# Performance work log

Measured on AMD Instinct MI355X. Metric: run time of the kernel, lower is better.

Reference implementation:

```python
import jax, jax.numpy as jnp
import numpy as np

COMMIT = 0.25
DECAY = 0.99
EPS = 1e-5
TEMP = 0.1
B, T, D, M = 32, 512, 256, 1024


def setup_inputs() -> dict:
    key = jax.random.key(0)
    k1, k2, k3 = jax.random.split(key, 3)
    init_bound = 1.0 / 400.0
    audio = jax.random.normal(k1, (B, T, D), jnp.float32)
    video = jax.random.normal(k2, (B, T, D), jnp.float32)
    embedding = jax.random.uniform(k3, (M, D), jnp.float32, -init_bound, init_bound)
    return {
        "audio_semantic": audio,
        "video_semantic": video,
        "embedding": embedding,
        "ema_count": jnp.zeros((M,), jnp.float32),
        "ema_weight": embedding,
        "epoch": 1,
    }


def reference(audio_semantic, video_semantic, embedding, ema_count, ema_weight, epoch):
    sg = jax.lax.stop_gradient
    Bc, Tc, Dc = audio_semantic.shape
    Mc = embedding.shape[0]

    a_flat = sg(audio_semantic.reshape(-1, Dc))  # [N, D], detached in torch
    v_flat = sg(video_semantic.reshape(-1, Dc))

    e_sq = jnp.sum(embedding ** 2, axis=1)  # [M]

    def sq_dist(x):
        return e_sq[None, :] + jnp.sum(x ** 2, axis=1, keepdims=True) - 2.0 * (x @ embedding.T)

    a_dist = sq_dist(a_flat)
    v_dist = sq_dist(v_flat)
    a_dist_g = sq_dist(audio_semantic.reshape(-1, Dc))  # grad-carrying copies
    v_dist_g = sq_dist(video_semantic.reshape(-1, Dc))

    # soft assignment probs and entropy-based adjustment
    a_ph = jax.nn.softmax(-jnp.sqrt(jnp.maximum(a_dist_g, 0.0)), axis=1)
    v_ph = jax.nn.softmax(-jnp.sqrt(jnp.maximum(v_dist_g, 0.0)), axis=1)
    entropy = lambda p: -jnp.sum(p * jnp.log(p + 1e-5), axis=-1)
    max_entropy = float(np.log(Mc))
    a_adj = (1.0 - entropy(a_ph) / max_entropy)[:, None]  # [N, 1]
    v_adj = (1.0 - entropy(v_ph) / max_entropy)[:, None]

    # hard assignment
    a_idx = jnp.argmin(a_dist, axis=-1)  # [N]
    v_idx = jnp.argmin(v_dist, axis=-1)
    a_onehot = jax.nn.one_hot(a_idx, Mc, dtype=jnp.float32)  # a_positive
    v_onehot = jax.nn.one_hot(v_idx, Mc, dtype=jnp.float32)  # v_positive
    a_enc = sg(a_adj * a_onehot)  # detached entropy-weighted encodings
    v_enc = sg(v_adj * v_onehot)

    # EMA update pass 1 (video-driven)
    ec = DECAY * ema_count + (1.0 - DECAY) * jnp.sum(v_enc, axis=0)
    n = jnp.sum(ec)
    ec = (ec + EPS) / (n + Mc * EPS) * n
    ew = DECAY * ema_weight + 0.5 * (1.0 - DECAY) * (v_enc.T @ (v_flat + a_flat))
    # EMA update pass 2 (audio-driven)
    ec = DECAY * ec + (1.0 - DECAY) * jnp.sum(a_enc, axis=0)
    n = jnp.sum(ec)
    ec = (ec + EPS) / (n + Mc * EPS) * n
    ew = DECAY * ew + 0.5 * (1.0 - DECAY) * (a_enc.T @ (a_flat + v_flat))
    emb_new = sg(ew / ec[:, None])  # updated codebook used by the contrastive loss

    en = emb_new / jnp.maximum(jnp.linalg.norm(emb_new, axis=1, keepdims=True), 1e-8)

    def info_nce(feats, self_pos, coupled_pos):
        fn = feats / jnp.maximum(jnp.linalg.norm(feats, axis=1, keepdims=True), 1e-8)
        logp = jax.nn.log_softmax((fn @ en.T) / TEMP, axis=1)  # [N, M]
        ce = lambda tgt: -jnp.mean(jnp.sum(tgt * logp, axis=1))
        return COMMIT * ce(self_pos) + (1.0 - COMMIT) * ce(coupled_pos)

    a_cpcl = info_nce(audio_semantic.reshape(-1, Dc), a_onehot, v_onehot)
    v_cpcl = info_nce(video_semantic.reshape(-1, Dc), v_onehot, a_onehot)
    cpcl_loss = (COMMIT * a_cpcl + COMMIT * v_cpcl) / Bc
    return cpcl_loss
```

## Files before the change

### kernel.cpp

```cpp
#include <hip/hip_runtime.h>
#include <math.h>

#define NROWS 16384
#define NR2 32768
#define DIM 256
#define MC 1024
#define GBM 128
#define GBK 64
#define NCHUNK 16

constexpr float kDecay = 0.99f;
constexpr float kEps = 1e-5f;
constexpr float kTemp = 0.1f;
constexpr float kCommit = 0.25f;
constexpr float kMaxEnt = 6.93147180559945f;

using short8 = __attribute__((ext_vector_type(8))) short;
using f32x4 = __attribute__((ext_vector_type(4))) float;

__device__ __forceinline__ float wave_sum(float v) {
#pragma unroll
  for (int off = 32; off > 0; off >>= 1) v += __shfl_xor(v, off);
  return v;
}

__device__ __forceinline__ unsigned short f2bf(float f) {
  union { float f; unsigned int u; } c;
  c.f = f;
  const unsigned int u = c.u;
  return (unsigned short)((u + 0x7FFFu + ((u >> 16) & 1u)) >> 16);
}
__device__ __forceinline__ float bf2f(unsigned short h) {
  union { unsigned int u; float f; } c;
  c.u = ((unsigned int)h) << 16;
  return c.f;
}

__global__ __launch_bounds__(256) void convert_all(const float* __restrict__ A,
                                                   const float* __restrict__ V,
                                                   const float* __restrict__ E,
                                                   unsigned short* __restrict__ av_bf,
                                                   unsigned short* __restrict__ e_bf,
                                                   float* __restrict__ xsq,
                                                   float* __restrict__ esq) {
  const int row = (int)((blockIdx.x * blockDim.x + threadIdx.x) >> 6);
  const int lane = threadIdx.x & 63;
  const float* src;
  unsigned short* dst;
  float* sqo;
  if (row < NR2) {
    src = (row < NROWS) ? (A + (size_t)row * DIM) : (V + (size_t)(row - NROWS) * DIM);
    dst = av_bf + (size_t)row * DIM;
    sqo = xsq + row;
  } else {
    const int r = row - NR2;
    src = E + (size_t)r * DIM;
    dst = e_bf + (size_t)r * DIM;
    sqo = esq + r;
  }
  const float4 x = *reinterpret_cast<const float4*>(src + (lane << 2));
  float s = x.x * x.x + x.y * x.y + x.z * x.z + x.w * x.w;
  ushort4 b;
  b.x = f2bf(x.x); b.y = f2bf(x.y); b.z = f2bf(x.z); b.w = f2bf(x.w);
  *reinterpret_cast<ushort4*>(dst + (lane << 2)) = b;
  s = wave_sum(s);
  if (lane == 0) *sqo = s;
}

__device__ __forceinline__ void stage_tile(const unsigned short* __restrict__ X,
                                           const unsigned short* __restrict__ W,
                                           char* lds, int k0, int row0, int col0, int w, int l) {
#pragma unroll
  for (int j = 0; j < 4; ++j) {
    const int sbase = __builtin_amdgcn_readfirstlane((w * 4 + j) * 1024);
    const int s = sbase + (l << 4);
    const int row = s >> 7;
    const int colb = s & 127;
    const int scolb = colb ^ ((row & 7) << 4);
    const char* srcA = (const char*)(X + (size_t)(row0 + row) * DIM + k0) + scolb;
    const char* srcB = (const char*)(W + (size_t)(col0 + row) * DIM + k0) + scolb;
    __builtin_amdgcn_global_load_lds(
        (const __attribute__((address_space(1))) unsigned int*)srcA,
        (__attribute__((address_space(3))) unsigned int*)(lds + sbase), 16, 0, 0);
    __builtin_amdgcn_global_load_lds(
        (const __attribute__((address_space(1))) unsigned int*)srcB,
        (__attribute__((address_space(3))) unsigned int*)(lds + 16384 + sbase), 16, 0, 0);
  }
}

__device__ __forceinline__ void mfma_step(const char* lds, f32x4 acc[4][4], int wr, int wc,
                                          int l) {
#pragma unroll
  for (int ks = 0; ks < 2; ++ks) {
    short8 af[4], bq[4];
    const int cb = ks * 64 + (l >> 4) * 16;
#pragma unroll
    for (int m = 0; m < 4; ++m) {
      const int ar = wr * 64 + m * 16 + (l & 15);
      af[m] = *reinterpret_cast<const short8*>(lds + ar * 128 + (cb ^ ((ar & 7) << 4)));
    }
#pragma unroll
    for (int n = 0; n < 4; ++n) {
      const int br = wc * 64 + n * 16 + (l & 15);
      bq[n] = *reinterpret_cast<const short8*>(lds + 16384 + br * 128 + (cb ^ ((br & 7) << 4)));
    }
#pragma unroll
    for (int m = 0; m < 4; ++m)
#pragma unroll
      for (int n = 0; n < 4; ++n)
        acc[m][n] = __builtin_amdgcn_mfma_f32_16x16x32_bf16(bq[n], af[m], acc[m][n], 0, 0, 0);
  }
}

__global__ __launch_bounds__(256, 4) void gemm_dist(const unsigned short* __restrict__ X,
                                                    const unsigned short* __restrict__ W,
                                                    const float* __restrict__ xsq,
                                                    const float* __restrict__ esq,
                                                    float4* __restrict__ pd4) {
  __shared__ __align__(16) char lds[32768 + 1024];
  float* esq_s = (float*)(lds + 32768);
  float* xsq_s = (float*)(lds + 32768 + 512);
  const int tid = threadIdx.x;
  const int l = tid & 63;
  const int w = tid >> 6;
  const int wr = w >> 1, wc = w & 1;
  int bid = blockIdx.y * 8 + blockIdx.x;
  bid = (bid & 7) * 256 + (bid >> 3);
  const int bx = bid & 7;
  const int by = bid >> 3;
  const int row0 = by * GBM;
  const int col0 = bx * GBM;
  if (tid < 128) esq_s[tid] = esq[col0 + tid];
  else xsq_s[tid - 128] = xsq[row0 + tid - 128];
  f32x4 acc[4][4] = {};
#pragma unroll
  for (int t = 0; t < 4; ++t) {
    stage_tile(X, W, lds, t * GBK, row0, col0, w, l);
    __syncthreads();
    mfma_step(lds, acc, wr, wc, l);
    if (t < 3) __syncthreads();
  }
  const int l15 = l & 15, lg = l >> 4;
  const int chunk = bx * 2 + wc;
#pragma unroll
  for (int m = 0; m < 4; ++m) {
    const float xs = xsq_s[wr * 64 + m * 16 + l15];
    float se = 0.f, wsabs = 0.f, bv = INFINITY;
    int bi = 0;
#pragma unroll
    for (int n = 0; n < 4; ++n) {
      const f32x4 es4 = *reinterpret_cast<const f32x4*>(&esq_s[wc * 64 + n * 16 + lg * 4]);
#pragma unroll
      for (int reg = 0; reg < 4; ++reg) {
        const float dist = fmaf(-2.0f, acc[m][n][reg], xs) + es4[reg];
        const int colg = col0 + wc * 64 + n * 16 + lg * 4 + reg;
        if (dist < bv) { bv = dist; bi = colg; }
        const float sabs = sqrtf(fmaxf(dist, 0.0f));
        const float e = __expf(-sabs);
        se += e;
        wsabs = fmaf(e, sabs, wsabs);
      }
    }
#pragma unroll
    for (int off = 16; off <= 32; off <<= 1) {
      se += __shfl_xor(se, off);
      wsabs += __shfl_xor(wsabs, off);
      const float obv = __shfl_xor(bv, off);
      const int obi = __shfl_xor(bi, off);
      if (obv < bv || (obv == bv && obi < bi)) { bv = obv; bi = obi; }
    }
    if (lg == 0) {
      const int grow = row0 + wr * 64 + m * 16 + l15;
      pd4[(size_t)chunk * NR2 + grow] = make_float4(se, -wsabs, bv, __int_as_float(bi));
    }
  }
}

__global__ __launch_bounds__(256) void dist_combine(const float4* __restrict__ pd4,
                                                    int* __restrict__ idx_out,
                                                    float* __restrict__ adj_out) {
  const int row = blockIdx.x * 256 + threadIdx.x;
  float SE = 0.f, WS = 0.f, BV = INFINITY;
  int BI = 0;
#pragma unroll
  for (int c = 0; c < NCHUNK; ++c) {
    const float4 st = pd4[(size_t)c * NR2 + row];
    SE += st.x;
    WS += st.y;
    if (st.z < BV) { BV = st.z; BI = __float_as_int(st.w); }
  }
  const float H = logf(SE) - WS / SE - 1e-5f * (float)MC;
  idx_out[row] = BI;
  adj_out[row] = 1.0f - H / kMaxEnt;
}

__global__ __launch_bounds__(256) void scatter_ema(const unsigned short* __restrict__ av,
                                                   const int* __restrict__ idx,
                                                   const float* __restrict__ adj,
                                                   float* __restrict__ acc_a,
                                                   float* __restrict__ acc_v,
                                                   float* __restrict__ cnt_a,
                                                   float* __restrict__ cnt_v) {
  const int row = blockIdx.x;
  const int d = threadIdx.x;
  const float s = bf2f(av[(size_t)row * DIM + d]) + bf2f(av[(size_t)(row + NROWS) * DIM + d]);
  const int ia = idx[row], iv = idx[row + NROWS];
  const float wa = adj[row], wv = adj[row + NROWS];
  atomicAdd(acc_a + (size_t)ia * DIM + d, wa * s);
  atomicAdd(acc_v + (size_t)iv * DIM + d, wv * s);
  if (d == 0) {
    atomicAdd(cnt_a + ia, wa);
    atomicAdd(cnt_v + iv, wv);
  }
}

__global__ __launch_bounds__(1024) void ec_kernel(const float* __restrict__ ema_count,
                                                  const float* __restrict__ cnt_v,
                                                  const float* __restrict__ cnt_a,
                                                  float* __restrict__ ec_out) {
  __shared__ float red[1024];
  const int m = threadIdx.x;
  float ec = kDecay * ema_count[m] + (1.f - kDecay) * cnt_v[m];
  red[m] = ec;
  __syncthreads();
  for (int s = 512; s > 0; s >>= 1) {
    if (m < s) red[m] += red[m + s];
    __syncthreads();
  }
  float n = red[0];
  __syncthreads();
  ec = (ec + kEps) / (n + MC * kEps) * n;
  ec = kDecay * ec + (1.f - kDecay) * cnt_a[m];
  red[m] = ec;
  __syncthreads();
  for (int s = 512; s > 0; s >>= 1) {
    if (m < s) red[m] += red[m + s];
    __syncthreads();
  }
  n = red[0];
  ec = (ec + kEps) / (n + MC * kEps) * n;
  ec_out[m] = ec;
}

__global__ __launch_bounds__(256) void en_kernel(const float* __restrict__ ema_weight,
                                                 const float* __restrict__ acc_v,
                                                 const float* __restrict__ acc_a,
                                                 const float* __restrict__ ec,
                                                 unsigned short* __restrict__ en_b) {
  const int mcode = blockIdx.x;
  const int d = threadIdx.x;
  const size_t o = (size_t)mcode * DIM + d;
  float ew = kDecay * ema_weight[o] + 0.5f * (1.f - kDecay) * acc_v[o];
  ew = kDecay * ew + 0.5f * (1.f - kDecay) * acc_a[o];
  const float e = ew / ec[mcode];
  __shared__ float red[256];
  red[d] = e * e;
  __syncthreads();
  for (int s = 128; s > 0; s >>= 1) {
    if (d < s) red[d] += red[d + s];
    __syncthreads();
  }
  const float nrm = sqrtf(red[0]);
  en_b[o] = f2bf(e / fmaxf(nrm, 1e-8f));
}

__global__ __launch_bounds__(256, 4) void gemm_nce(const unsigned short* __restrict__ X,
                                                   const unsigned short* __restrict__ W,
                                                   const float* __restrict__ xsq,
                                                   float* __restrict__ pn) {
  __shared__ __align__(16) char lds[32768 + 512];
  float* xsq_s = (float*)(lds + 32768);
  const int tid = threadIdx.x;
  const int l = tid & 63;
  const int w = tid >> 6;
  const int wr = w >> 1, wc = w & 1;
  int bid = blockIdx.y * 8 + blockIdx.x;
  bid = (bid & 7) * 256 + (bid >> 3);
  const int bx = bid & 7;
  const int by = bid >> 3;
  const int row0 = by * GBM;
  const int col0 = bx * GBM;
  if (tid < 128) xsq_s[tid] = xsq[row0 + tid];
  f32x4 acc[4][4] = {};
#pragma unroll
  for (int t = 0; t < 4; ++t) {
    stage_tile(X, W, lds, t * GBK, row0, col0, w, l);
    __syncthreads();
    mfma_step(lds, acc, wr, wc, l);
    if (t < 3) __syncthreads();
  }
  const int l15 = l & 15, lg = l >> 4;
  const int chunk = bx * 2 + wc;
#pragma unroll
  for (int m = 0; m < 4; ++m) {
    const float xs = xsq_s[wr * 64 + m * 16 + l15];
    const float inv = 10.0f * rsqrtf(fmaxf(xs, 1e-16f));
    float se = 0.f;
#pragma unroll
    for (int n = 0; n < 4; ++n)
#pragma unroll
      for (int reg = 0; reg < 4; ++reg) se += __expf(acc[m][n][reg] * inv);
    se += __shfl_xor(se, 16);
    se += __shfl_xor(se, 32);
    if (lg == 0) pn[(size_t)chunk * NR2 + (row0 + wr * 64 + m * 16 + l15)] = se;
  }
}

__global__ __launch_bounds__(256) void nce_combine(const float* __restrict__ pn,
                                                   const unsigned short* __restrict__ av_bf,
                                                   const unsigned short* __restrict__ en_bf,
                                                   const float* __restrict__ xsq,
                                                   const int* __restrict__ idx,
                                                   float* __restrict__ part) {
  __shared__ float sp[8];
  const int row = (int)((blockIdx.x * blockDim.x + threadIdx.x) >> 6);
  const int lane = threadIdx.x & 63;
  const int wib = threadIdx.x >> 6;
  const float m = (lane < NCHUNK) ? pn[(size_t)lane * NR2 + row] : 0.f;
  const float SE = wave_sum(m);
  const float lse = logf(SE);
  const int si = idx[row], ci = idx[row ^ NROWS];
  const ushort4 x4 = *reinterpret_cast<const ushort4*>(av_bf + (size_t)row * DIM + (lane << 2));
  const ushort4 s4 = *reinterpret_cast<const ushort4*>(en_bf + (size_t)si * DIM + (lane << 2));
  const ushort4 c4 = *reinterpret_cast<const ushort4*>(en_bf + (size_t)ci * DIM + (lane << 2));
  float ds = bf2f(x4.x) * bf2f(s4.x) + bf2f(x4.y) * bf2f(s4.y) + bf2f(x4.z) * bf2f(s4.z) +
             bf2f(x4.w) * bf2f(s4.w);
  float dc = bf2f(x4.x) * bf2f(c4.x) + bf2f(x4.y) * bf2f(c4.y) + bf2f(x4.z) * bf2f(c4.z) +
             bf2f(x4.w) * bf2f(c4.w);
  ds = wave_sum(ds);
  dc = wave_sum(dc);
  const float inv = 1.0f / (fmaxf(sqrtf(xsq[row]), 1e-8f) * kTemp);
  if (lane == 0) {
    sp[wib] = ds * inv - lse;
    sp[4 + wib] = dc * inv - lse;
  }
  __syncthreads();
  if (threadIdx.x == 0) {
    part[blockIdx.x] = sp[0] + sp[1] + sp[2] + sp[3];
    part[8192 + blockIdx.x] = sp[4] + sp[5] + sp[6] + sp[7];
  }
}

__global__ __launch_bounds__(1024) void finalize(const float* __restrict__ part,
                                                 float* __restrict__ out) {
  const int tid = threadIdx.x;
  const int lane = tid & 63;
  const int wid = tid >> 6;
  float ss = 0.f, sc = 0.f;
  for (int i = tid; i < 8192; i += 1024) {
    ss += part[i];
    sc += part[8192 + i];
  }
  ss = wave_sum(ss);
  sc = wave_sum(sc);
  __shared__ float red[16][2];
  if (lane == 0) { red[wid][0] = ss; red[wid][1] = sc; }
  __syncthreads();
  if (tid == 0) {
    float t0 = 0.f, t1 = 0.f;
#pragma unroll
    for (int i = 0; i < 16; ++i) { t0 += red[i][0]; t1 += red[i][1]; }
    out[0] = -(kCommit / (32.0f * (float)NROWS)) * (kCommit * t0 + (1.f - kCommit) * t1);
  }
}

extern "C" void kernel_launch(void* const* d_in, const int* in_sizes, int n_in, void* d_out,
                              int out_size, void* d_ws, size_t ws_size, hipStream_t stream) {
  const float* audio = (const float*)d_in[0];
  const float* video = (const float*)d_in[1];
  const float* emb = (const float*)d_in[2];
  const float* ema_count = (const float*)d_in[3];
  const float* ema_weight = (const float*)d_in[4];
  float* out = (float*)d_out;

  float* ws = (float*)d_ws;
  size_t off = 0;
  float4* pd4 = (float4*)(ws + off); off += (size_t)NCHUNK * NR2 * 4;
  float* pn = ws + off; off += (size_t)NCHUNK * NR2;
  float* esq = ws + off; off += MC;
  float* xsq = ws + off; off += NR2;
  float* adj = ws + off; off += NR2;
  int* idx = (int*)(ws + off); off += NR2;
  float* cnt_a = ws + off; off += MC;
  float* cnt_v = ws + off; off += MC;
  float* acc_a = ws + off; off += (size_t)MC * DIM;
  float* acc_v = ws + off; off += (size_t)MC * DIM;
  float* ec = ws + off; off += MC;
  float* part = ws + off; off += 16384;
  unsigned short* av_bf = (unsigned short*)(ws + off); off += (size_t)NR2 * DIM / 2;
  unsigned short* e_bf = (unsigned short*)(ws + off); off += (size_t)MC * DIM / 2;
  unsigned short* en_bf = (unsigned short*)(ws + off); off += (size_t)MC * DIM / 2;

  hipMemsetAsync(cnt_a, 0, (size_t)(2 * MC + 2 * (size_t)MC * DIM) * sizeof(float), stream);

  const dim3 b256(256);
  const dim3 ggrid(MC / GBM, NR2 / GBM);

  convert_all<<<(NR2 + MC) / 4, b256, 0, stream>>>(audio, video, emb, av_bf, e_bf, xsq, esq);

  gemm_dist<<<ggrid, b256, 0, stream>>>(av_bf, e_bf, xsq, esq, pd4);
  dist_combine<<<NR2 / 256, b256, 0, stream>>>(pd4, idx, adj);

  scatter_ema<<<NROWS, b256, 0, stream>>>(av_bf, idx, adj, acc_a, acc_v, cnt_a, cnt_v);
  ec_kernel<<<1, 1024, 0, stream>>>(ema_count, cnt_v, cnt_a, ec);
  en_kernel<<<MC, b256, 0, stream>>>(ema_weight, acc_v, acc_a, ec, en_bf);

  gemm_nce<<<ggrid, b256, 0, stream>>>(av_bf, en_bf, xsq, pn);
  nce_combine<<<NR2 / 4, b256, 0, stream>>>(pn, av_bf, en_bf, xsq, idx, part);

  finalize<<<1, 1024, 0, stream>>>(part, out);
}
```

Measured before the change: 209.9 us.

## Fuse distance combine into scatter and extract target logits inside NCE GEMM

Merges dist_combine into scatter_ema so each block reduces its two rows' chunk partials with wave shuffles before doing the atomic EMA accumulation. This removes one launch and the adj round trip. gemm_nce now writes the self and coupled logits directly when a column matches the row's index, replacing the separate gathered dot products in nce_combine with a thread-per-row reduction. The final reduction shrinks to a single 64-thread wave. Costs are extra compare/store work in the GEMM epilogue, an idx load per row there, and a combine_scatter that serialises the chunk reduction ahead of the atomics in every block.

```diff
diff --git a/kernel.cpp b/kernel.cpp
--- a/kernel.cpp
+++ b/kernel.cpp
@@ -176,36 +176,41 @@
   }
 }
 
-__global__ __launch_bounds__(256) void dist_combine(const float4* __restrict__ pd4,
-                                                    int* __restrict__ idx_out,
-                                                    float* __restrict__ adj_out) {
-  const int row = blockIdx.x * 256 + threadIdx.x;
-  float SE = 0.f, WS = 0.f, BV = INFINITY;
-  int BI = 0;
-#pragma unroll
-  for (int c = 0; c < NCHUNK; ++c) {
+__global__ __launch_bounds__(256) void combine_scatter(
+    const float4* __restrict__ pd4, const unsigned short* __restrict__ av,
+    int* __restrict__ idx_out, float* __restrict__ acc_a, float* __restrict__ acc_v,
+    float* __restrict__ cnt_a, float* __restrict__ cnt_v) {
+  __shared__ int sidx[2];
+  __shared__ float sadj[2];
+  const int r = blockIdx.x;
+  const int tid = threadIdx.x;
+  if (tid < 32) {
+    const int which = tid >> 4;
+    const int c = tid & 15;
+    const int row = r + which * NROWS;
     const float4 st = pd4[(size_t)c * NR2 + row];
-    SE += st.x;
-    WS += st.y;
-    if (st.z < BV) { BV = st.z; BI = __float_as_int(st.w); }
-  }
-  const float H = logf(SE) - WS / SE - 1e-5f * (float)MC;
-  idx_out[row] = BI;
-  adj_out[row] = 1.0f - H / kMaxEnt;
-}
-
-__global__ __launch_bounds__(256) void scatter_ema(const unsigned short* __restrict__ av,
-                                                   const int* __restrict__ idx,
-                                                   const float* __restrict__ adj,
-                                                   float* __restrict__ acc_a,
-                                                   float* __restrict__ acc_v,
-                                                   float* __restrict__ cnt_a,
-                                                   float* __restrict__ cnt_v) {
-  const int row = blockIdx.x;
-  const int d = threadIdx.x;
-  const float s = bf2f(av[(size_t)row * DIM + d]) + bf2f(av[(size_t)(row + NROWS) * DIM + d]);
-  const int ia = idx[row], iv = idx[row + NROWS];
-  const float wa = adj[row], wv = adj[row + NROWS];
+    float SE = st.x, WS = st.y, BV = st.z;
+    int BI = __float_as_int(st.w);
+#pragma unroll
+    for (int off = 1; off < 16; off <<= 1) {
+      SE += __shfl_xor(SE, off);
+      WS += __shfl_xor(WS, off);
+      const float obv = __shfl_xor(BV, off);
+      const int obi = __shfl_xor(BI, off);
+      if (obv < BV || (obv == BV && obi < BI)) { BV = obv; BI = obi; }
+    }
+    if (c == 0) {
+      const float H = logf(SE) - WS / SE - 1e-5f * (float)MC;
+      sidx[which] = BI;
+      sadj[which] = 1.0f - H / kMaxEnt;
+      idx_out[row] = BI;
+    }
+  }
+  __syncthreads();
+  const int ia = sidx[0], iv = sidx[1];
+  const float wa = sadj[0], wv = sadj[1];
+  const int d = tid;
+  const float s = bf2f(av[(size_t)r * DIM + d]) + bf2f(av[(size_t)(r + NROWS) * DIM + d]);
   atomicAdd(acc_a + (size_t)ia * DIM + d, wa * s);
   atomicAdd(acc_v + (size_t)iv * DIM + d, wv * s);
   if (d == 0) {
@@ -267,7 +272,10 @@
 __global__ __launch_bounds__(256, 4) void gemm_nce(const unsigned short* __restrict__ X,
                                                    const unsigned short* __restrict__ W,
                                                    const float* __restrict__ xsq,
-                                                   float* __restrict__ pn) {
+                                                   const int* __restrict__ idx,
+                                                   float* __restrict__ pn,
+                                                   float* __restrict__ pself,
+                                                   float* __restrict__ pcoup) {
   __shared__ __align__(16) char lds[32768 + 512];
   float* xsq_s = (float*)(lds + 32768);
   const int tid = threadIdx.x;
@@ -291,77 +299,67 @@
   }
   const int l15 = l & 15, lg = l >> 4;
   const int chunk = bx * 2 + wc;
+  const int cbase = col0 + wc * 64 + lg * 4;
 #pragma unroll
   for (int m = 0; m < 4; ++m) {
+    const int grow = row0 + wr * 64 + m * 16 + l15;
     const float xs = xsq_s[wr * 64 + m * 16 + l15];
     const float inv = 10.0f * rsqrtf(fmaxf(xs, 1e-16f));
+    const int si = idx[grow];
+    const int ci = idx[grow ^ NROWS];
     float se = 0.f;
 #pragma unroll
     for (int n = 0; n < 4; ++n)
 #pragma unroll
-      for (int reg = 0; reg < 4; ++reg) se += __expf(acc[m][n][reg] * inv);
+      for (int reg = 0; reg < 4; ++reg) {
+        const float lv = acc[m][n][reg] * inv;
+        se += __expf(lv);
+        const int colg = cbase + n * 16 + reg;
+        if (colg == si) pself[grow] = lv;
+        if (colg == ci) pcoup[grow] = lv;
+      }
     se += __shfl_xor(se, 16);
     se += __shfl_xor(se, 32);
-    if (lg == 0) pn[(size_t)chunk * NR2 + (row0 + wr * 64 + m * 16 + l15)] = se;
-  }
-}
-
-__global__ __launch_bounds__(256) void nce_combine(const float* __restrict__ pn,
-                                                   const unsigned short* __restrict__ av_bf,
-                                                   const unsigned short* __restrict__ en_bf,
-                                                   const float* __restrict__ xsq,
-                                                   const int* __restrict__ idx,
-                                                   float* __restrict__ part) {
+    if (lg == 0) pn[(size_t)chunk * NR2 + grow] = se;
+  }
+}
+
+__global__ __launch_bounds__(256) void nce_reduce(const float* __restrict__ pn,
+                                                  const float* __restrict__ pself,
+                                                  const float* __restrict__ pcoup,
+                                                  float* __restrict__ part) {
   __shared__ float sp[8];
-  const int row = (int)((blockIdx.x * blockDim.x + threadIdx.x) >> 6);
+  const int row = blockIdx.x * 256 + threadIdx.x;
   const int lane = threadIdx.x & 63;
   const int wib = threadIdx.x >> 6;
-  const float m = (lane < NCHUNK) ? pn[(size_t)lane * NR2 + row] : 0.f;
-  const float SE = wave_sum(m);
+  float SE = 0.f;
+#pragma unroll
+  for (int c = 0; c < NCHUNK; ++c) SE += pn[(size_t)c * NR2 + row];
   const float lse = logf(SE);
-  const int si = idx[row], ci = idx[row ^ NROWS];
-  const ushort4 x4 = *reinterpret_cast<const ushort4*>(av_bf + (size_t)row * DIM + (lane << 2));
-  const ushort4 s4 = *reinterpret_cast<const ushort4*>(en_bf + (size_t)si * DIM + (lane << 2));
-  const ushort4 c4 = *reinterpret_cast<const ushort4*>(en_bf + (size_t)ci * DIM + (lane << 2));
-  float ds = bf2f(x4.x) * bf2f(s4.x) + bf2f(x4.y) * bf2f(s4.y) + bf2f(x4.z) * bf2f(s4.z) +
-             bf2f(x4.w) * bf2f(s4.w);
-  float dc = bf2f(x4.x) * bf2f(c4.x) + bf2f(x4.y) * bf2f(c4.y) + bf2f(x4.z) * bf2f(c4.z) +
-             bf2f(x4.w) * bf2f(c4.w);
-  ds = wave_sum(ds);
-  dc = wave_sum(dc);
-  const float inv = 1.0f / (fmaxf(sqrtf(xsq[row]), 1e-8f) * kTemp);
+  float ps = pself[row] - lse;
+  float pc = pcoup[row] - lse;
+  ps = wave_sum(ps);
+  pc = wave_sum(pc);
   if (lane == 0) {
-    sp[wib] = ds * inv - lse;
-    sp[4 + wib] = dc * inv - lse;
+    sp[wib] = ps;
+    sp[4 + wib] = pc;
   }
   __syncthreads();
   if (threadIdx.x == 0) {
     part[blockIdx.x] = sp[0] + sp[1] + sp[2] + sp[3];
-    part[8192 + blockIdx.x] = sp[4] + sp[5] + sp[6] + sp[7];
-  }
-}
-
-__global__ __launch_bounds__(1024) void finalize(const float* __restrict__ part,
-                                                 float* __restrict__ out) {
-  const int tid = threadIdx.x;
-  const int lane = tid & 63;
-  const int wid = tid >> 6;
-  float ss = 0.f, sc = 0.f;
-  for (int i = tid; i < 8192; i += 1024) {
-    ss += part[i];
-    sc += part[8192 + i];
-  }
+    part[128 + blockIdx.x] = sp[4] + sp[5] + sp[6] + sp[7];
+  }
+}
+
+__global__ __launch_bounds__(64) void finalize(const float* __restrict__ part,
+                                               float* __restrict__ out) {
+  const int l = threadIdx.x;
+  float ss = part[l] + part[l + 64];
+  float sc = part[128 + l] + part[192 + l];
   ss = wave_sum(ss);
   sc = wave_sum(sc);
-  __shared__ float red[16][2];
-  if (lane == 0) { red[wid][0] = ss; red[wid][1] = sc; }
-  __syncthreads();
-  if (tid == 0) {
-    float t0 = 0.f, t1 = 0.f;
-#pragma unroll
-    for (int i = 0; i < 16; ++i) { t0 += red[i][0]; t1 += red[i][1]; }
-    out[0] = -(kCommit / (32.0f * (float)NROWS)) * (kCommit * t0 + (1.f - kCommit) * t1);
-  }
+  if (l == 0)
+    out[0] = -(kCommit / (32.0f * (float)NROWS)) * (kCommit * ss + (1.f - kCommit) * sc);
 }
 
 extern "C" void kernel_launch(void* const* d_in, const int* in_sizes, int n_in, void* d_out,
@@ -377,16 +375,17 @@
   size_t off = 0;
   float4* pd4 = (float4*)(ws + off); off += (size_t)NCHUNK * NR2 * 4;
   float* pn = ws + off; off += (size_t)NCHUNK * NR2;
+  float* pself = ws + off; off += NR2;
+  float* pcoup = ws + off; off += NR2;
   float* esq = ws + off; off += MC;
   float* xsq = ws + off; off += NR2;
-  float* adj = ws + off; off += NR2;
   int* idx = (int*)(ws + off); off += NR2;
   float* cnt_a = ws + off; off += MC;
   float* cnt_v = ws + off; off += MC;
   float* acc_a = ws + off; off += (size_t)MC * DIM;
   float* acc_v = ws + off; off += (size_t)MC * DIM;
   float* ec = ws + off; off += MC;
-  float* part = ws + off; off += 16384;
+  float* part = ws + off; off += 256;
   unsigned short* av_bf = (unsigned short*)(ws + off); off += (size_t)NR2 * DIM / 2;
   unsigned short* e_bf = (unsigned short*)(ws + off); off += (size_t)MC * DIM / 2;
   unsigned short* en_bf = (unsigned short*)(ws + off); off += (size_t)MC * DIM / 2;
@@ -399,14 +398,13 @@
   convert_all<<<(NR2 + MC) / 4, b256, 0, stream>>>(audio, video, emb, av_bf, e_bf, xsq, esq);
 
   gemm_dist<<<ggrid, b256, 0, stream>>>(av_bf, e_bf, xsq, esq, pd4);
-  dist_combine<<<NR2 / 256, b256, 0, stream>>>(pd4, idx, adj);
-
-  scatter_ema<<<NROWS, b256, 0, stream>>>(av_bf, idx, adj, acc_a, acc_v, cnt_a, cnt_v);
+  combine_scatter<<<NROWS, b256, 0, stream>>>(pd4, av_bf, idx, acc_a, acc_v, cnt_a, cnt_v);
+
   ec_kernel<<<1, 1024, 0, stream>>>(ema_count, cnt_v, cnt_a, ec);
   en_kernel<<<MC, b256, 0, stream>>>(ema_weight, acc_v, acc_a, ec, en_bf);
 
-  gemm_nce<<<ggrid, b256, 0, stream>>>(av_bf, en_bf, xsq, pn);
-  nce_combine<<<NR2 / 4, b256, 0, stream>>>(pn, av_bf, en_bf, xsq, idx, part);
-
-  finalize<<<1, 1024, 0, stream>>>(part, out);
-}
+  gemm_nce<<<ggrid, b256, 0, stream>>>(av_bf, en_bf, xsq, idx, pn, pself, pcoup);
+  nce_reduce<<<NR2 / 256, b256, 0, stream>>>(pn, pself, pcoup, part);
+
+  finalize<<<1, 64, 0, stream>>>(part, out);
+}
```

Result: faster. 201.4 us (-4.0%).
